# Kernel optimization log

Measured on AMD Instinct MI355X. Metric: run time of the kernel, lower is better.

## Reference

```python
import jax, jax.numpy as jnp
import numpy as np

N_NODES = 100000
N_EDGES = 3200000
F_IN = 128
F_OUT = 16


def setup_inputs() -> dict:
    key = jax.random.key(0)
    k1, k2, k3, k4, k5 = jax.random.split(key, 5)
    x = jax.random.normal(k1, (N_NODES, F_IN), dtype=jnp.float32)
    edge_index = jax.random.randint(k2, (2, N_EDGES), 0, N_NODES, dtype=jnp.int64)
    edge_weights = jax.random.uniform(k3, (N_EDGES,), dtype=jnp.float32)
    W = jax.random.normal(k4, (F_IN, F_OUT), dtype=jnp.float32) / np.sqrt(F_IN)
    b = jax.random.normal(k5, (F_OUT,), dtype=jnp.float32)
    return {"x": x, "edge_index": edge_index, "edge_weights": edge_weights, "W": W, "b": b}


def reference(x, edge_index, edge_weights, W, b):
    # GCNConv: out = D^{-1/2} (A + I) D^{-1/2} X W + b  (weighted edges, self-loops)
    n = x.shape[0]
    row = edge_index[0]  # source nodes
    col = edge_index[1]  # target nodes (aggregation destination)
    # add self-loops with weight 1.0 (GCNConv default)
    loop = jnp.arange(n, dtype=row.dtype)
    row_f = jnp.concatenate([row, loop])
    col_f = jnp.concatenate([col, loop])
    ew = jnp.concatenate([edge_weights, jnp.ones((n,), dtype=edge_weights.dtype)])
    # symmetric normalization: deg over destination, norm = d^{-1/2}[row] * w * d^{-1/2}[col]
    deg = jax.ops.segment_sum(ew, col_f, num_segments=n)
    dinv = jnp.where(deg > 0, jax.lax.rsqrt(deg), 0.0)
    norm = dinv[row_f] * ew * dinv[col_f]  # [E+N]
    h = x @ W  # [N, F_OUT] dense projection before propagation
    msgs = h[row_f] * norm[:, None]  # gather + scale, [E+N, F_OUT]
    out = jax.ops.segment_sum(msgs, col_f, num_segments=n)  # scatter-add
    return out + b
```

## Files before the change

### kernel.cpp

```cpp
#include <hip/hip_runtime.h>

#define N_NODES 100000
#define N_EDGES 3200000
#define F_IN 128
#define F_OUT 16

#define NSEG 512
#define EPS (N_EDGES / NSEG)
#define EPT 13
#define NBUCK 512
#define NPB 196
#define CAPR 7424
#define GEMM32 ((N_NODES + 31) / 32)
#define PULL_BLOCKS 2048

#define OFF_CUR   0x000000u
#define OFF_NPTR  0x010000u
#define OFF_NCNT  0x080000u
#define OFF_DINV  0x0F0000u
#define OFF_HH    0x160000u
#define OFF_GG    0x780000u
#define OFF_CSR   0xB00000u
#define WS_NEEDED ((size_t)0x1000000 + (size_t)N_EDGES * 8)

__device__ __forceinline__ unsigned short f2bf(float f) {
    unsigned u = __float_as_uint(f);
    unsigned r = (u + 0x7FFFu + ((u >> 16) & 1u)) >> 16;
    return (unsigned short)r;
}
__device__ __forceinline__ float bf2f(unsigned short v) {
    return __uint_as_float((unsigned)v << 16);
}


__global__ void __launch_bounds__(512) k_binA(const int* __restrict__ row,
                                              const int* __restrict__ col,
                                              const float* __restrict__ ew,
                                              int* __restrict__ cursor,
                                              int2* __restrict__ csr,
                                              const float* __restrict__ x,
                                              const float* __restrict__ W,
                                              float* __restrict__ h) {
    __shared__ int smem[2048];
    int tid = threadIdx.x;
    if (blockIdx.x < NSEG) {
        int* lcnt = smem;
        int* gofs = smem + 512;
        int e0 = blockIdx.x * EPS;
        lcnt[tid] = 0;
        __syncthreads();

        int2 rec[EPT];
        int meta[EPT];
#pragma unroll
        for (int k = 0; k < EPT; ++k) {
            int i = k * 512 + tid;
            if (k < EPT - 1 || i < EPS) {
                int e = e0 + i;
                int r = row[e];
                int c = col[e];
                float w = ew[e];
                int bk = c / NPB;
                int pos = atomicAdd(&lcnt[bk], 1);
                rec[k] = make_int2((r << 8) | (c - bk * NPB), __float_as_int(w));
                meta[k] = (bk << 16) | pos;
            }
        }
        __syncthreads();

        int v = lcnt[tid];
        gofs[tid] = tid * CAPR + atomicAdd(&cursor[tid], v);
        __syncthreads();

#pragma unroll
        for (int k = 0; k < EPT; ++k) {
            int i = k * 512 + tid;
            if (k < EPT - 1 || i < EPS) {
                int m = meta[k];
                csr[gofs[m >> 16] + (m & 0xFFFF)] = rec[k];
            }
        }
    } else {
        float* Ws = (float*)smem;
        for (int i = tid; i < F_IN * F_OUT; i += 512) Ws[i] = W[i];
        __syncthreads();
        int n = (blockIdx.x - NSEG) * 32 + (tid >> 4);
        int j = tid & 15;
        if (n >= N_NODES) return;
        const float4* xr = (const float4*)(x + (size_t)n * F_IN);
        float acc = 0.0f;
#pragma unroll
        for (int k4 = 0; k4 < F_IN / 4; ++k4) {
            float4 xv = xr[k4];
            int k = k4 * 4;
            acc += xv.x * Ws[(k + 0) * F_OUT + j];
            acc += xv.y * Ws[(k + 1) * F_OUT + j];
            acc += xv.z * Ws[(k + 2) * F_OUT + j];
            acc += xv.w * Ws[(k + 3) * F_OUT + j];
        }
        h[(size_t)n * F_OUT + j] = acc;
    }
}

__global__ void __launch_bounds__(256) k_sortA(const int* __restrict__ cursor,
                                               int2* __restrict__ csr,
                                               const float* __restrict__ h,
                                               float* __restrict__ dinv,
                                               unsigned short* __restrict__ gb,
                                               int* __restrict__ nodeptr,
                                               int* __restrict__ ncnt) {
    __shared__ int2 srec[CAPR];
    __shared__ unsigned short spos[CAPR];
    __shared__ int cnt[256];
    __shared__ int basel[256];
    __shared__ int wtot[4];
    __shared__ float dl[256];
    int tid = threadIdx.x;
    int b = blockIdx.x;
    int c0 = b * NPB;
    int rb = b * CAPR;
    int total = cursor[b];
    if (total > CAPR) total = CAPR;

    cnt[tid] = 0;
    __syncthreads();
    for (int i = tid; i < total; i += 256) {
        int2 rec = csr[rb + i];
        srec[i] = rec;
        spos[i] = (unsigned short)atomicAdd(&cnt[rec.x & 255], 1);
    }
    __syncthreads();

    int v = cnt[tid];
    int inc = v;
#pragma unroll
    for (int off = 1; off < 64; off <<= 1) {
        int t = __shfl_up(inc, off);
        if ((tid & 63) >= off) inc += t;
    }
    if ((tid & 63) == 63) wtot[tid >> 6] = inc;
    __syncthreads();
    int woff = 0;
#pragma unroll
    for (int k = 0; k < 4; ++k)
        if (k < (tid >> 6)) woff += wtot[k];
    int excl = woff + inc - v;
    int n = c0 + tid;
    if (tid < NPB && n < N_NODES) {
        nodeptr[n] = rb + excl;
        ncnt[n] = v;
    }
    basel[tid] = excl;
    __syncthreads();

    for (int i = tid; i < total; i += 256) {
        int2 rec = srec[i];
        int p = basel[rec.x & 255] + spos[i];
        csr[rb + p] = make_int2(rec.x >> 8, rec.y);
    }
    __syncthreads();

    float d = 0.0f;
    if (tid < NPB && n < N_NODES) {
        float s = 1.0f;
        const int2* run = csr + rb + excl;
        for (int k = 0; k < v; ++k) s += __int_as_float(run[k].y);
        d = rsqrtf(s);
        dinv[n] = d;
    }
    dl[tid] = d;
    __syncthreads();
    for (int i = tid; i < NPB * F_OUT; i += 256) {
        int idx = c0 * F_OUT + i;
        if (idx < N_NODES * F_OUT) gb[idx] = f2bf(dl[i >> 4] * h[idx]);
    }
}

__global__ void __launch_bounds__(256) k_pull4(const int* __restrict__ nodeptr,
                                               const int* __restrict__ ncnt,
                                               const int2* __restrict__ csr,
                                               const unsigned short* __restrict__ gb,
                                               const float* __restrict__ dinv,
                                               const float* __restrict__ bias,
                                               float* __restrict__ out) {
    int wid = threadIdx.x >> 6;
    int lane = threadIdx.x & 63;
    int l4 = lane & 15;
    int fr = ((l4 & 1) << 3) | ((l4 & 2) << 1) | ((l4 & 4) >> 1) | ((l4 & 8) >> 3);
    float bj = bias[fr];
    for (int n = blockIdx.x * 4 + wid; n < N_NODES; n += PULL_BLOCKS * 4) {
        int p0 = nodeptr[n];
        int c = ncnt[n];
        float acc[16];
#pragma unroll
        for (int k = 0; k < 16; ++k) acc[k] = 0.0f;
        for (int base = 0; base < c; base += 64) {
            int i = base + lane;
            int2 rec = (i < c) ? csr[p0 + i] : make_int2(0, 0);
            float w = __int_as_float(rec.y);
            const uint4* gr = (const uint4*)(gb + ((size_t)rec.x << 4));
            uint4 qa = gr[0];
            uint4 qb = gr[1];
            acc[0]  += w * __uint_as_float(qa.x << 16);
            acc[1]  += w * __uint_as_float(qa.x & 0xFFFF0000u);
            acc[2]  += w * __uint_as_float(qa.y << 16);
            acc[3]  += w * __uint_as_float(qa.y & 0xFFFF0000u);
            acc[4]  += w * __uint_as_float(qa.z << 16);
            acc[5]  += w * __uint_as_float(qa.z & 0xFFFF0000u);
            acc[6]  += w * __uint_as_float(qa.w << 16);
            acc[7]  += w * __uint_as_float(qa.w & 0xFFFF0000u);
            acc[8]  += w * __uint_as_float(qb.x << 16);
            acc[9]  += w * __uint_as_float(qb.x & 0xFFFF0000u);
            acc[10] += w * __uint_as_float(qb.y << 16);
            acc[11] += w * __uint_as_float(qb.y & 0xFFFF0000u);
            acc[12] += w * __uint_as_float(qb.z << 16);
            acc[13] += w * __uint_as_float(qb.z & 0xFFFF0000u);
            acc[14] += w * __uint_as_float(qb.w << 16);
            acc[15] += w * __uint_as_float(qb.w & 0xFFFF0000u);
        }
        bool b1 = (lane & 1) != 0;
#pragma unroll
        for (int k = 0; k < 8; ++k) {
            float keep = b1 ? acc[k + 8] : acc[k];
            float send = b1 ? acc[k] : acc[k + 8];
            acc[k] = keep + __shfl_xor(send, 1);
        }
        bool b2 = (lane & 2) != 0;
#pragma unroll
        for (int k = 0; k < 4; ++k) {
            float keep = b2 ? acc[k + 4] : acc[k];
            float send = b2 ? acc[k] : acc[k + 4];
            acc[k] = keep + __shfl_xor(send, 2);
        }
        bool b4 = (lane & 4) != 0;
#pragma unroll
        for (int k = 0; k < 2; ++k) {
            float keep = b4 ? acc[k + 2] : acc[k];
            float send = b4 ? acc[k] : acc[k + 2];
            acc[k] = keep + __shfl_xor(send, 4);
        }
        bool b8 = (lane & 8) != 0;
        {
            float keep = b8 ? acc[1] : acc[0];
            float send = b8 ? acc[0] : acc[1];
            acc[0] = keep + __shfl_xor(send, 8);
        }
        acc[0] += __shfl_xor(acc[0], 16);
        acc[0] += __shfl_xor(acc[0], 32);
        if (lane < 16) {
            float d = dinv[n];
            float gs = bf2f(gb[(size_t)n * F_OUT + fr]);
            out[(size_t)n * F_OUT + fr] = bj + d * (gs + acc[0]);
        }
    }
}


#define EDGE_BLOCKS_FB ((N_EDGES + 255) / 256)
#define GEMM_BLOCKS_FB ((N_NODES + 15) / 16)
__global__ void k_init_fb(float* __restrict__ deg) {
    int i = blockIdx.x * blockDim.x + threadIdx.x;
    if (i < N_NODES) deg[i] = 1.0f;
}
__global__ void k_fused_fb(const int* __restrict__ col, const float* __restrict__ ew,
                           float* __restrict__ deg, const float* __restrict__ x,
                           const float* __restrict__ W, float* __restrict__ h) {
    int b3 = blockIdx.x / 3;
    int r3 = blockIdx.x % 3;
    if (r3 < 2) {
        int e = (b3 * 2 + r3) * 256 + threadIdx.x;
        if (e < N_EDGES) atomicAdd(&deg[col[e]], ew[e]);
    } else {
        __shared__ float Ws[F_IN * F_OUT];
        int tid = threadIdx.x;
        for (int i = tid; i < F_IN * F_OUT; i += 256) Ws[i] = W[i];
        __syncthreads();
        int n = b3 * 16 + (tid >> 4);
        int j = tid & 15;
        if (n >= N_NODES) return;
        const float4* xr = (const float4*)(x + (size_t)n * F_IN);
        float acc = 0.0f;
#pragma unroll
        for (int k4 = 0; k4 < F_IN / 4; ++k4) {
            float4 xv = xr[k4];
            int k = k4 * 4;
            acc += xv.x * Ws[(k + 0) * F_OUT + j];
            acc += xv.y * Ws[(k + 1) * F_OUT + j];
            acc += xv.z * Ws[(k + 2) * F_OUT + j];
            acc += xv.w * Ws[(k + 3) * F_OUT + j];
        }
        h[(size_t)n * F_OUT + j] = acc;
    }
}
__global__ void k_final_fb(float* __restrict__ deg, const float* __restrict__ h,
                           const float* __restrict__ b, float* __restrict__ g,
                           float* __restrict__ out) {
    int i = blockIdx.x * blockDim.x + threadIdx.x;
    int n = i >> 4;
    int j = i & 15;
    if (n >= N_NODES) return;
    float d = rsqrtf(deg[n]);
    if (j == 0) deg[n] = d;
    float gg = d * h[i];
    g[i] = gg;
    out[i] = b[j] + d * gg;
}
__global__ void k_scatter_fb(const int* __restrict__ row, const int* __restrict__ col,
                             const float* __restrict__ ew, const float* __restrict__ dinv,
                             const float* __restrict__ g, float* __restrict__ out) {
    long long tid = (long long)blockIdx.x * blockDim.x + threadIdx.x;
    int e = (int)(tid >> 4);
    int j = (int)(tid & 15);
    if (e >= N_EDGES) return;
    int c = col[e];
    float norm = ew[e] * dinv[c];
    atomicAdd(&out[(size_t)c * F_OUT + j], g[(size_t)row[e] * F_OUT + j] * norm);
}

extern "C" void kernel_launch(void* const* d_in, const int* in_sizes, int n_in,
                              void* d_out, int out_size, void* d_ws, size_t ws_size,
                              hipStream_t stream) {
    const float* x  = (const float*)d_in[0];
    const int*   ei = (const int*)d_in[1];
    const float* ew = (const float*)d_in[2];
    const float* W  = (const float*)d_in[3];
    const float* b  = (const float*)d_in[4];
    float* out = (float*)d_out;

    const int* row = ei;
    const int* col = ei + N_EDGES;

    char* ws = (char*)d_ws;
    dim3 blk(256);

    if (ws_size >= WS_NEEDED) {
        int*   cur  = (int*)(ws + OFF_CUR);
        int*   nptr = (int*)(ws + OFF_NPTR);
        int*   ncnt = (int*)(ws + OFF_NCNT);
        float* dinv = (float*)(ws + OFF_DINV);
        float* h    = (float*)(ws + OFF_HH);
        unsigned short* gb = (unsigned short*)(ws + OFF_GG);
        int2*  csr  = (int2*)(ws + OFF_CSR);

        hipMemsetAsync(cur, 0, NBUCK * sizeof(int), stream);
        k_binA<<<NSEG + GEMM32, 512, 0, stream>>>(row, col, ew, cur, csr, x, W, h);
        k_sortA<<<NBUCK, blk, 0, stream>>>(cur, csr, h, dinv, gb, nptr, ncnt);
        k_pull4<<<PULL_BLOCKS, blk, 0, stream>>>(nptr, ncnt, csr, gb, dinv, b, out);
    } else {
        float* deg = (float*)ws;
        float* h   = (float*)(ws + (1u << 20));
        float* g   = (float*)(ws + (8u << 20));
        k_init_fb<<<(N_NODES + 255) / 256, blk, 0, stream>>>(deg);
        k_fused_fb<<<EDGE_BLOCKS_FB + GEMM_BLOCKS_FB, blk, 0, stream>>>(col, ew, deg, x, W, h);
        k_final_fb<<<(N_NODES * F_OUT + 255) / 256, blk, 0, stream>>>(deg, h, b, g, out);
        long long total = (long long)N_EDGES * F_OUT;
        k_scatter_fb<<<(unsigned)((total + 255) / 256), blk, 0, stream>>>(row, col, ew, deg, g, out);
    }
}
```

Before: 239.4 us.

## Stage bucketed edges in LDS for coalesced writes; keep sort records in registers

The binning kernel now does a local prefix sum over bucket counts and first reorders each segment's edges in shared memory by bucket. It then writes them out contiguously, so the global scatter becomes mostly coalesced runs instead of random 8-byte stores. The sort kernel keeps records and positions in registers (29 per thread) instead of large shared arrays, which reduces LDS use and may raise occupancy. The cost is a much larger shared-memory footprint in k_binB, about 55KB, which also applies to the GEMM blocks sharing the kernel, plus higher register pressure in k_sortB.

```diff
diff --git a/kernel.cpp b/kernel.cpp
--- a/kernel.cpp
+++ b/kernel.cpp
@@ -11,6 +11,7 @@
 #define NBUCK 512
 #define NPB 196
 #define CAPR 7424
+#define RPT 29
 #define GEMM32 ((N_NODES + 31) / 32)
 #define PULL_BLOCKS 2048
 
@@ -33,7 +34,7 @@
 }
 
 
-__global__ void __launch_bounds__(512) k_binA(const int* __restrict__ row,
+__global__ void __launch_bounds__(512) k_binB(const int* __restrict__ row,
                                               const int* __restrict__ col,
                                               const float* __restrict__ ew,
                                               int* __restrict__ cursor,
@@ -41,11 +42,14 @@
                                               const float* __restrict__ x,
                                               const float* __restrict__ W,
                                               float* __restrict__ h) {
-    __shared__ int smem[2048];
+    __shared__ int2 srec[EPS];
+    __shared__ unsigned char sbk[EPS];
+    __shared__ int lcnt[NBUCK];
+    __shared__ int lpre[NBUCK];
+    __shared__ int gofs[NBUCK];
+    __shared__ int wtot[8];
     int tid = threadIdx.x;
     if (blockIdx.x < NSEG) {
-        int* lcnt = smem;
-        int* gofs = smem + 512;
         int e0 = blockIdx.x * EPS;
         lcnt[tid] = 0;
         __syncthreads();
@@ -69,19 +73,42 @@
         __syncthreads();
 
         int v = lcnt[tid];
-        gofs[tid] = tid * CAPR + atomicAdd(&cursor[tid], v);
-        __syncthreads();
-
+        int inc = v;
+#pragma unroll
+        for (int off = 1; off < 64; off <<= 1) {
+            int t = __shfl_up(inc, off);
+            if ((tid & 63) >= off) inc += t;
+        }
+        if ((tid & 63) == 63) wtot[tid >> 6] = inc;
+        __syncthreads();
+        int woff = 0;
+#pragma unroll
+        for (int k = 0; k < 8; ++k)
+            if (k < (tid >> 6)) woff += wtot[k];
+        int excl = woff + inc - v;
+        lpre[tid] = excl;
+        gofs[tid] = tid * CAPR + atomicAdd(&cursor[tid], v) - excl;
+        __syncthreads();
+
+        int mid = lpre[256];
 #pragma unroll
         for (int k = 0; k < EPT; ++k) {
             int i = k * 512 + tid;
             if (k < EPT - 1 || i < EPS) {
                 int m = meta[k];
-                csr[gofs[m >> 16] + (m & 0xFFFF)] = rec[k];
+                int slot = lpre[m >> 16] + (m & 0xFFFF);
+                srec[slot] = rec[k];
+                sbk[slot] = (unsigned char)(m >> 16);
             }
         }
+        __syncthreads();
+
+        for (int t = tid; t < EPS; t += 512) {
+            int bk = sbk[t] + ((t >= mid) ? 256 : 0);
+            csr[gofs[bk] + t] = srec[t];
+        }
     } else {
-        float* Ws = (float*)smem;
+        float* Ws = (float*)srec;
         for (int i = tid; i < F_IN * F_OUT; i += 512) Ws[i] = W[i];
         __syncthreads();
         int n = (blockIdx.x - NSEG) * 32 + (tid >> 4);
@@ -102,15 +129,13 @@
     }
 }
 
-__global__ void __launch_bounds__(256) k_sortA(const int* __restrict__ cursor,
+__global__ void __launch_bounds__(256) k_sortB(const int* __restrict__ cursor,
                                                int2* __restrict__ csr,
                                                const float* __restrict__ h,
                                                float* __restrict__ dinv,
                                                unsigned short* __restrict__ gb,
                                                int* __restrict__ nodeptr,
                                                int* __restrict__ ncnt) {
-    __shared__ int2 srec[CAPR];
-    __shared__ unsigned short spos[CAPR];
     __shared__ int cnt[256];
     __shared__ int basel[256];
     __shared__ int wtot[4];
@@ -124,10 +149,16 @@
 
     cnt[tid] = 0;
     __syncthreads();
-    for (int i = tid; i < total; i += 256) {
-        int2 rec = csr[rb + i];
-        srec[i] = rec;
-        spos[i] = (unsigned short)atomicAdd(&cnt[rec.x & 255], 1);
+
+    int2 rec[RPT];
+    int pos[RPT];
+#pragma unroll
+    for (int k = 0; k < RPT; ++k) {
+        int i = k * 256 + tid;
+        if (i < total) {
+            rec[k] = csr[rb + i];
+            pos[k] = atomicAdd(&cnt[rec[k].x & 255], 1);
+        }
     }
     __syncthreads();
 
@@ -153,10 +184,13 @@
     basel[tid] = excl;
     __syncthreads();
 
-    for (int i = tid; i < total; i += 256) {
-        int2 rec = srec[i];
-        int p = basel[rec.x & 255] + spos[i];
-        csr[rb + p] = make_int2(rec.x >> 8, rec.y);
+#pragma unroll
+    for (int k = 0; k < RPT; ++k) {
+        int i = k * 256 + tid;
+        if (i < total) {
+            int cl = rec[k].x & 255;
+            csr[rb + basel[cl] + pos[k]] = make_int2(rec[k].x >> 8, rec[k].y);
+        }
     }
     __syncthreads();
 
@@ -343,8 +377,8 @@
         int2*  csr  = (int2*)(ws + OFF_CSR);
 
         hipMemsetAsync(cur, 0, NBUCK * sizeof(int), stream);
-        k_binA<<<NSEG + GEMM32, 512, 0, stream>>>(row, col, ew, cur, csr, x, W, h);
-        k_sortA<<<NBUCK, blk, 0, stream>>>(cur, csr, h, dinv, gb, nptr, ncnt);
+        k_binB<<<NSEG + GEMM32, 512, 0, stream>>>(row, col, ew, cur, csr, x, W, h);
+        k_sortB<<<NBUCK, blk, 0, stream>>>(cur, csr, h, dinv, gb, nptr, ncnt);
         k_pull4<<<PULL_BLOCKS, blk, 0, stream>>>(nptr, ncnt, csr, gb, dinv, b, out);
     } else {
         float* deg = (float*)ws;
```

Result: no change. 240.1 us (+0.3%).
